# Optimization experiments

Hardware: AMD Instinct MI355X
Metric: run time of the kernel (lower is better)

Reference implementation:

```python
import jax, jax.numpy as jnp
import numpy as np

MARGIN = 0.3


def setup_inputs() -> dict:
    key = jax.random.key(0)
    k1, k2 = jax.random.split(key)
    B, D, N_IDS = 8192, 256, 512
    emb = jax.random.normal(k1, (B, D), dtype=jnp.float32)
    emb = emb / jnp.linalg.norm(emb, axis=1, keepdims=True)  # L2-normalized as docstring states
    labels = jax.random.randint(k2, (B,), 0, N_IDS, dtype=jnp.int64)
    return {"embeddings": emb, "labels": labels}


def reference(embeddings, labels):
    B = embeddings.shape[0]
    # pairwise Euclidean distance via cosine similarity (embeddings are L2-normalized)
    sim = jnp.matmul(embeddings, embeddings.T)              # (B, B)
    dist = jnp.sqrt(jnp.clip(2.0 - 2.0 * sim, 0.0) + 1e-12)
    same = labels[:, None] == labels[None, :]               # (B, B)
    eye = jnp.eye(B, dtype=bool)
    pos_mask = same & ~eye
    neg_mask = ~same
    neg_inf = jnp.asarray(-jnp.inf, dist.dtype)
    pos_inf = jnp.asarray(jnp.inf, dist.dtype)
    dist_ap = jnp.max(jnp.where(pos_mask, dist, neg_inf), axis=1)  # hardest positive per anchor
    dist_an = jnp.min(jnp.where(neg_mask, dist, pos_inf), axis=1)  # hardest negative per anchor
    valid = jnp.any(pos_mask, axis=1) & jnp.any(neg_mask, axis=1)
    # MarginRankingLoss(dist_an, dist_ap, y=1) = mean(relu(dist_ap - dist_an + margin)) over valid anchors
    per = jnp.maximum(dist_ap - dist_an + MARGIN, 0.0)
    per = jnp.where(valid, per, 0.0)
    n_valid = jnp.sum(valid.astype(dist.dtype))
    loss = jnp.where(n_valid > 0, jnp.sum(per) / jnp.maximum(n_valid, 1.0), 0.0)
    return loss
```

## Files before the change

### kernel.cpp

```cpp
#include <hip/hip_runtime.h>
#include <hip/hip_bf16.h>


#define BDIM 8192
#define DDIM 256

typedef short bf16x8 __attribute__((ext_vector_type(8)));
typedef float f32x4  __attribute__((ext_vector_type(4)));
typedef unsigned short u16;

static __device__ __forceinline__ bf16x8 ld_frag(const u16* p) {
    return *reinterpret_cast<const bf16x8*>(p);
}

static __device__ __forceinline__ u16 f2bf(float f) {
    union { float f; unsigned int u; } x; x.f = f;
    unsigned int u = x.u;
    unsigned int r = u + 0x7fffu + ((u >> 16) & 1u);
    return (u16)(r >> 16);
}

static __device__ __forceinline__ void gload_lds16(const u16* g, u16* l) {
    __builtin_amdgcn_global_load_lds(
        (const __attribute__((address_space(1))) unsigned int*)g,
        (__attribute__((address_space(3))) unsigned int*)l, 16, 0, 0);
}

__global__ __launch_bounds__(256) void cvt_init_kernel(const float* __restrict__ in,
                                                       u16* __restrict__ out,
                                                       int* __restrict__ minpos,
                                                       int* __restrict__ maxneg) {
    int i = blockIdx.x * 256 + threadIdx.x;
    const float4 v = reinterpret_cast<const float4*>(in)[i];
    ushort4 o;
    o.x = f2bf(v.x); o.y = f2bf(v.y); o.z = f2bf(v.z); o.w = f2bf(v.w);
    reinterpret_cast<ushort4*>(out)[i] = o;
    if (i < BDIM) {
        minpos[i] = 0x7f800000;
        maxneg[i] = 0;
    }
}

__global__ __launch_bounds__(256, 2) void triplet_main(const u16* __restrict__ Ebf,
                                                       const int* __restrict__ labels,
                                                       int* __restrict__ minpos,
                                                       int* __restrict__ maxneg) {
    __shared__ __align__(16) u16 smem[2][64 * DDIM];
    __shared__ int slab[512];

    const int tid  = threadIdx.x;
    const int w    = tid >> 6;
    const int l    = tid & 63;
    const int quad = l >> 4;
    const int r16  = l & 15;

    const int mblk  = blockIdx.x * 256 + w * 64;
    const int nbase = blockIdx.y * 512;

    slab[tid]       = labels[nbase + tid];
    slab[256 + tid] = labels[nbase + 256 + tid];

    bf16x8 a[4][8];
#pragma unroll
    for (int ms = 0; ms < 4; ++ms) {
        const u16* ap = Ebf + (size_t)(mblk + ms * 16 + r16) * DDIM + quad * 8;
#pragma unroll
        for (int k = 0; k < 8; ++k) a[ms][k] = ld_frag(ap + k * 32);
    }

    int lab_row[4][4];
#pragma unroll
    for (int ms = 0; ms < 4; ++ms)
#pragma unroll
        for (int r = 0; r < 4; ++r)
            lab_row[ms][r] = labels[mblk + ms * 16 + quad * 4 + r];

    float minp[4][4], maxn[4][4];
#pragma unroll
    for (int ms = 0; ms < 4; ++ms)
#pragma unroll
        for (int r = 0; r < 4; ++r) { minp[ms][r] = __builtin_inff(); maxn[ms][r] = -__builtin_inff(); }

    const int qs = quad ^ (r16 & 3);
    const int s4 = (r16 >> 2) & 1;

    auto stage = [&](int t, int buf) {
        const int n1 = nbase + t * 64;
#pragma unroll
        for (int it = 0; it < 8; ++it) {
            const int q = it * 256 + tid;
            const int r = q >> 5;
            const int c = (q & 31) ^ (r & 7);
            gload_lds16(Ebf + ((size_t)(n1 + r) << 8) + c * 8,
                        &smem[buf][0] + it * 2048 + w * 512);
        }
    };

    stage(0, 0);

#pragma unroll 1
    for (int t = 0; t < 8; ++t) {
        const int cur = t & 1;
        const int n0  = nbase + t * 64;

        asm volatile("s_waitcnt vmcnt(0) lgkmcnt(0)" ::: "memory");
        __builtin_amdgcn_s_barrier();
        __builtin_amdgcn_sched_barrier(0);

        if (t + 1 < 8) stage(t + 1, cur ^ 1);

        int lab_c[4];
#pragma unroll
        for (int nt = 0; nt < 4; ++nt) lab_c[nt] = slab[t * 64 + nt * 16 + r16];

        f32x4 acc[4][4];
#pragma unroll
        for (int ms = 0; ms < 4; ++ms)
#pragma unroll
            for (int nt = 0; nt < 4; ++nt)
                acc[ms][nt] = (f32x4){0.f, 0.f, 0.f, 0.f};

        const u16* bb = &smem[cur][0];

        __builtin_amdgcn_s_setprio(1);
#pragma unroll
        for (int nt = 0; nt < 4; ++nt) {
            const u16* bp = bb + (nt * 16 + r16) * DDIM + qs * 8;
#pragma unroll
            for (int k = 0; k < 8; ++k) {
                const bf16x8 b = ld_frag(bp + ((k ^ s4) << 5));
#pragma unroll
                for (int ms = 0; ms < 4; ++ms)
                    acc[ms][nt] = __builtin_amdgcn_mfma_f32_16x16x32_bf16(
                        a[ms][k], b, acc[ms][nt], 0, 0, 0);
            }
        }
        __builtin_amdgcn_s_setprio(0);

        const bool diagTile = (n0 < mblk + 64) && (mblk < n0 + 64);
        if (__builtin_expect(diagTile, 0)) {
#pragma unroll
            for (int nt = 0; nt < 4; ++nt) {
                const int colg = n0 + nt * 16 + r16;
#pragma unroll
                for (int ms = 0; ms < 4; ++ms)
#pragma unroll
                    for (int r = 0; r < 4; ++r) {
                        const int rowg = mblk + ms * 16 + quad * 4 + r;
                        const float s = acc[ms][nt][r];
                        const bool same = (lab_c[nt] == lab_row[ms][r]);
                        const bool pos  = same && (colg != rowg);
                        minp[ms][r] = fminf(minp[ms][r], pos  ?  s : __builtin_inff());
                        maxn[ms][r] = fmaxf(maxn[ms][r], same ? -__builtin_inff() : s);
                    }
            }
        } else {
#pragma unroll
            for (int nt = 0; nt < 4; ++nt)
#pragma unroll
                for (int ms = 0; ms < 4; ++ms)
#pragma unroll
                    for (int r = 0; r < 4; ++r) {
                        const float s = acc[ms][nt][r];
                        const bool same = (lab_c[nt] == lab_row[ms][r]);
                        minp[ms][r] = fminf(minp[ms][r], same ?  s : __builtin_inff());
                        maxn[ms][r] = fmaxf(maxn[ms][r], same ? -__builtin_inff() : s);
                    }
        }
    }

#pragma unroll
    for (int mask = 1; mask <= 8; mask <<= 1) {
#pragma unroll
        for (int ms = 0; ms < 4; ++ms)
#pragma unroll
            for (int r = 0; r < 4; ++r) {
                minp[ms][r] = fminf(minp[ms][r], __shfl_xor(minp[ms][r], mask, 64));
                maxn[ms][r] = fmaxf(maxn[ms][r], __shfl_xor(maxn[ms][r], mask, 64));
            }
    }
    if (r16 == 0) {
#pragma unroll
        for (int ms = 0; ms < 4; ++ms)
#pragma unroll
            for (int r = 0; r < 4; ++r) {
                const int rowg = mblk + ms * 16 + quad * 4 + r;
                atomicMin(minpos + rowg, __float_as_int(minp[ms][r] + 2.0f));
                atomicMax(maxneg + rowg, __float_as_int(maxn[ms][r] + 2.0f));
            }
    }
}

__global__ __launch_bounds__(1024) void finalize_kernel(const int* __restrict__ minpos,
                                                        const int* __restrict__ maxneg,
                                                        float* __restrict__ out) {
    __shared__ float ssum[16], scnt[16];
    float sum = 0.f, cnt = 0.f;
#pragma unroll
    for (int it = 0; it < 8; ++it) {
        const int i = it * 1024 + threadIdx.x;
        const float mp = __int_as_float(minpos[i]);
        const float mn = __int_as_float(maxneg[i]);
        if (mp < 1e30f && mn > 0.5f) {
            const float dap = sqrtf(fmaxf(6.0f - 2.0f * mp, 0.0f) + 1e-12f);
            const float dan = sqrtf(fmaxf(6.0f - 2.0f * mn, 0.0f) + 1e-12f);
            sum += fmaxf(dap - dan + 0.3f, 0.0f);
            cnt += 1.0f;
        }
    }
#pragma unroll
    for (int off = 32; off > 0; off >>= 1) {
        sum += __shfl_down(sum, off, 64);
        cnt += __shfl_down(cnt, off, 64);
    }
    const int wid = threadIdx.x >> 6;
    if ((threadIdx.x & 63) == 0) { ssum[wid] = sum; scnt[wid] = cnt; }
    __syncthreads();
    if (threadIdx.x == 0) {
        float S = 0.f, C = 0.f;
#pragma unroll
        for (int i = 0; i < 16; ++i) { S += ssum[i]; C += scnt[i]; }
        out[0] = (C > 0.f) ? (S / C) : 0.f;
    }
}

extern "C" void kernel_launch(void* const* d_in, const int* in_sizes, int n_in,
                              void* d_out, int out_size, void* d_ws, size_t ws_size,
                              hipStream_t stream) {
    const float* emb    = (const float*)d_in[0];
    const int*   labels = (const int*)d_in[1];
    float*       out    = (float*)d_out;

    u16* Ebf    = (u16*)d_ws;
    int* minpos = (int*)((char*)d_ws + (size_t)BDIM * DDIM * 2);
    int* maxneg = minpos + BDIM;

    cvt_init_kernel<<<dim3((BDIM * DDIM / 4) / 256), dim3(256), 0, stream>>>(emb, Ebf, minpos, maxneg);
    triplet_main<<<dim3(BDIM / 256, BDIM / 512), dim3(256), 0, stream>>>(Ebf, labels, minpos, maxneg);
    finalize_kernel<<<dim3(1), dim3(1024), 0, stream>>>(minpos, maxneg, out);
}
```

Before: 121.4 us.

## Give each wave private double-buffered B tiles to drop workgroup barriers

Each wave now stages its own 16-column slice of the B operand into a private LDS double buffer and iterates 32 times over 16 columns instead of 8 times over 64. This removes the workgroup-wide s_barrier and the full vmcnt(0) wait, replacing them with a per-wave vmcnt(8) wait that overlaps the next load. The cost is that each wave fetches all B columns itself, quadrupling global-to-LDS traffic. Each iteration also has fewer MFMAs to hide latency behind.

Measured after the change: 115.9 us. 1.05x faster.

```diff
diff --git a/kernel.cpp b/kernel.cpp
--- a/kernel.cpp
+++ b/kernel.cpp
@@ -45,7 +45,7 @@
                                                        const int* __restrict__ labels,
                                                        int* __restrict__ minpos,
                                                        int* __restrict__ maxneg) {
-    __shared__ __align__(16) u16 smem[2][64 * DDIM];
+    __shared__ __align__(16) u16 smem[4][2][16 * DDIM];
     __shared__ int slab[512];
 
     const int tid  = threadIdx.x;
@@ -81,91 +81,82 @@
 #pragma unroll
         for (int r = 0; r < 4; ++r) { minp[ms][r] = __builtin_inff(); maxn[ms][r] = -__builtin_inff(); }
 
+    __syncthreads();
+
     const int qs = quad ^ (r16 & 3);
     const int s4 = (r16 >> 2) & 1;
 
+    u16* const myLds = &smem[w][0][0];
     auto stage = [&](int t, int buf) {
-        const int n1 = nbase + t * 64;
+        const int n1 = nbase + t * 16;
 #pragma unroll
         for (int it = 0; it < 8; ++it) {
-            const int q = it * 256 + tid;
+            const int q = it * 64 + l;
             const int r = q >> 5;
             const int c = (q & 31) ^ (r & 7);
             gload_lds16(Ebf + ((size_t)(n1 + r) << 8) + c * 8,
-                        &smem[buf][0] + it * 2048 + w * 512);
+                        myLds + buf * (16 * DDIM) + it * 512);
         }
     };
 
     stage(0, 0);
 
 #pragma unroll 1
-    for (int t = 0; t < 8; ++t) {
+    for (int t = 0; t < 32; ++t) {
         const int cur = t & 1;
-        const int n0  = nbase + t * 64;
-
-        asm volatile("s_waitcnt vmcnt(0) lgkmcnt(0)" ::: "memory");
-        __builtin_amdgcn_s_barrier();
+
+        if (t + 1 < 32) {
+            stage(t + 1, cur ^ 1);
+            asm volatile("s_waitcnt vmcnt(8)" ::: "memory");
+        } else {
+            asm volatile("s_waitcnt vmcnt(0)" ::: "memory");
+        }
         __builtin_amdgcn_sched_barrier(0);
 
-        if (t + 1 < 8) stage(t + 1, cur ^ 1);
-
-        int lab_c[4];
-#pragma unroll
-        for (int nt = 0; nt < 4; ++nt) lab_c[nt] = slab[t * 64 + nt * 16 + r16];
-
-        f32x4 acc[4][4];
-#pragma unroll
-        for (int ms = 0; ms < 4; ++ms)
-#pragma unroll
-            for (int nt = 0; nt < 4; ++nt)
-                acc[ms][nt] = (f32x4){0.f, 0.f, 0.f, 0.f};
-
-        const u16* bb = &smem[cur][0];
+        const int n0    = nbase + t * 16;
+        const int lab_c = slab[t * 16 + r16];
+
+        f32x4 acc[4];
+#pragma unroll
+        for (int ms = 0; ms < 4; ++ms) acc[ms] = (f32x4){0.f, 0.f, 0.f, 0.f};
+
+        const u16* bp = myLds + cur * (16 * DDIM) + r16 * DDIM + qs * 8;
 
         __builtin_amdgcn_s_setprio(1);
 #pragma unroll
-        for (int nt = 0; nt < 4; ++nt) {
-            const u16* bp = bb + (nt * 16 + r16) * DDIM + qs * 8;
-#pragma unroll
-            for (int k = 0; k < 8; ++k) {
-                const bf16x8 b = ld_frag(bp + ((k ^ s4) << 5));
-#pragma unroll
-                for (int ms = 0; ms < 4; ++ms)
-                    acc[ms][nt] = __builtin_amdgcn_mfma_f32_16x16x32_bf16(
-                        a[ms][k], b, acc[ms][nt], 0, 0, 0);
-            }
+        for (int k = 0; k < 8; ++k) {
+            const bf16x8 b = ld_frag(bp + ((k ^ s4) << 5));
+#pragma unroll
+            for (int ms = 0; ms < 4; ++ms)
+                acc[ms] = __builtin_amdgcn_mfma_f32_16x16x32_bf16(
+                    a[ms][k], b, acc[ms], 0, 0, 0);
         }
         __builtin_amdgcn_s_setprio(0);
 
-        const bool diagTile = (n0 < mblk + 64) && (mblk < n0 + 64);
+        const bool diagTile = (n0 < mblk + 64) && (mblk < n0 + 16);
         if (__builtin_expect(diagTile, 0)) {
-#pragma unroll
-            for (int nt = 0; nt < 4; ++nt) {
-                const int colg = n0 + nt * 16 + r16;
-#pragma unroll
-                for (int ms = 0; ms < 4; ++ms)
-#pragma unroll
-                    for (int r = 0; r < 4; ++r) {
-                        const int rowg = mblk + ms * 16 + quad * 4 + r;
-                        const float s = acc[ms][nt][r];
-                        const bool same = (lab_c[nt] == lab_row[ms][r]);
-                        const bool pos  = same && (colg != rowg);
-                        minp[ms][r] = fminf(minp[ms][r], pos  ?  s : __builtin_inff());
-                        maxn[ms][r] = fmaxf(maxn[ms][r], same ? -__builtin_inff() : s);
-                    }
-            }
+            const int colg = n0 + r16;
+#pragma unroll
+            for (int ms = 0; ms < 4; ++ms)
+#pragma unroll
+                for (int r = 0; r < 4; ++r) {
+                    const int rowg = mblk + ms * 16 + quad * 4 + r;
+                    const float s = acc[ms][r];
+                    const bool same = (lab_c == lab_row[ms][r]);
+                    const bool pos  = same && (colg != rowg);
+                    minp[ms][r] = fminf(minp[ms][r], pos  ?  s : __builtin_inff());
+                    maxn[ms][r] = fmaxf(maxn[ms][r], same ? -__builtin_inff() : s);
+                }
         } else {
 #pragma unroll
-            for (int nt = 0; nt < 4; ++nt)
-#pragma unroll
-                for (int ms = 0; ms < 4; ++ms)
-#pragma unroll
-                    for (int r = 0; r < 4; ++r) {
-                        const float s = acc[ms][nt][r];
-                        const bool same = (lab_c[nt] == lab_row[ms][r]);
-                        minp[ms][r] = fminf(minp[ms][r], same ?  s : __builtin_inff());
-                        maxn[ms][r] = fmaxf(maxn[ms][r], same ? -__builtin_inff() : s);
-                    }
+            for (int ms = 0; ms < 4; ++ms)
+#pragma unroll
+                for (int r = 0; r < 4; ++r) {
+                    const float s = acc[ms][r];
+                    const bool same = (lab_c == lab_row[ms][r]);
+                    minp[ms][r] = fminf(minp[ms][r], same ?  s : __builtin_inff());
+                    maxn[ms][r] = fmaxf(maxn[ms][r], same ? -__builtin_inff() : s);
+                }
         }
     }
 
```
